# Performance work log

Measured on AMD Instinct MI355X. Metric: run time of the kernel, lower is better.

The kernel has to match this reference:

```python
import jax, jax.numpy as jnp
import numpy as np

B, N, F_NODE = 16, 48, 5
H1, H2 = 32, 64
D_ATT = H2 * 3  # 192


def setup_inputs() -> dict:
    rng = np.random.default_rng(0)
    n_nodes = B * N
    # complete graph per batch element; each directed pair appears with class 0 and class 1,
    # ordered by (src, dst, class) so that filtering src>dst leaves a sorted list where
    # consecutive rows are the (class0, class1) pair of the same undirected edge.
    i, j = np.meshgrid(np.arange(N), np.arange(N), indexing="ij")
    m = i != j
    pi = np.repeat(i[m], 2)
    pj = np.repeat(j[m], 2)
    cls = np.tile(np.array([0.0, 1.0], np.float32), N * (N - 1))
    offs = np.arange(B)[:, None] * N
    src = (pi[None] + offs).ravel()
    dst = (pj[None] + offs).ravel()
    edges = jnp.asarray(np.stack([src, dst]).astype(np.int64))
    w = rng.random(src.shape[0]).astype(np.float32)
    edge_attr = jnp.asarray(np.stack([w, np.tile(cls, B)], axis=1))
    x = jnp.asarray(rng.standard_normal((n_nodes, F_NODE)).astype(np.float32))
    detector_labels = jnp.ones((n_nodes,), bool)
    batch_labels = jnp.asarray(np.repeat(np.arange(B), N).astype(np.int64))

    def lin(k_out, k_in):
        s = 1.0 / np.sqrt(k_in)
        return (jnp.asarray(rng.uniform(-s, s, (k_out, k_in)).astype(np.float32)),
                jnp.asarray(rng.uniform(-s, s, (k_out,)).astype(np.float32)))

    W_we, b_we = lin(1, 3)
    Wrel1, brel1 = lin(H1, F_NODE); Wroot1, _ = lin(H1, F_NODE)
    Wrel2, brel2 = lin(H2, H1);     Wroot2, _ = lin(H2, H1)
    W_ee, b_ee = lin(H2, 3)
    W_qkv, b_qkv = lin(3 * D_ATT, D_ATT)
    W_in, b_in = lin(3 * D_ATT, D_ATT)
    W_out, b_out = lin(D_ATT, D_ATT)
    W_o, b_o = lin(1, D_ATT)
    return dict(x=x, edges=edges, edge_attr=edge_attr,
                detector_labels=detector_labels, batch_labels=batch_labels,
                W_we=W_we, b_we=b_we, Wrel1=Wrel1, brel1=brel1, Wroot1=Wroot1,
                Wrel2=Wrel2, brel2=brel2, Wroot2=Wroot2,
                W_ee=W_ee, b_ee=b_ee, W_qkv=W_qkv, b_qkv=b_qkv,
                W_in=W_in, b_in=b_in, W_out=W_out, b_out=b_out,
                W_o=W_o, b_o=b_o)


def _graph_conv(x, src, dst, w, Wrel, brel, Wroot, n_nodes):
    # pyg GraphConv: lin_rel(sum_{j->i} e_ji * x_j) + lin_root(x_i)
    msg = x[src] * w  # w: [E,1] scalar edge weight
    agg = jax.ops.segment_sum(msg, dst, num_segments=n_nodes)
    return agg @ Wrel.T + brel + x @ Wroot.T


def reference(x, edges, edge_attr, detector_labels, batch_labels,
              W_we, b_we, Wrel1, brel1, Wroot1, Wrel2, brel2, Wroot2,
              W_ee, b_ee, W_qkv, b_qkv, W_in, b_in, W_out, b_out, W_o, b_o):
    n_nodes = x.shape[0]
    E = edges.shape[1]
    src, dst = edges[0], edges[1]
    # edge weight embedding from (weight, one_hot(class))
    c = jax.nn.one_hot(edge_attr[:, 1].astype(jnp.int32), 2, dtype=x.dtype)
    w = jax.nn.relu(jnp.concatenate([edge_attr[:, :1], c], -1) @ W_we.T + b_we)  # [E,1]
    x = jax.nn.relu(_graph_conv(x, src, dst, w, Wrel1, brel1, Wroot1, n_nodes))
    x = jax.nn.relu(_graph_conv(x, src, dst, w, Wrel2, brel2, Wroot2, n_nodes))
    # keep one direction (src > dst): construction guarantees exactly E//2 kept, already sorted
    keep = jnp.nonzero(src > dst, size=E // 2)[0]
    srcK, dstK, ea = src[keep], dst[keep], edge_attr[keep]
    c = jax.nn.one_hot(ea[:, 1].astype(jnp.int32), 2, dtype=x.dtype)
    wK = jax.nn.relu(jnp.concatenate([ea[:, :1], c], -1) @ W_ee.T + b_ee)  # [Ek,H2]
    feat = jnp.concatenate([x[srcK], wK, x[dstK]], -1)  # [Ek, 3*H2]
    # equal-size graphs -> unbatch + pad_sequence == reshape (no padding)
    S = feat.shape[0] // B
    feat = feat.reshape(B, S, -1)
    e_src = srcK.reshape(B, S)
    e_dst = dstK.reshape(B, S)
    classes = ea[:, 1].reshape(B, S, 1)
    pad_mask = e_src == e_dst  # all False (no ragged padding here)
    # SelfAttention: extra qkv projection, then 1-head MultiheadAttention
    qkv = feat @ W_qkv.T + b_qkv
    q, k, v = jnp.split(qkv, 3, -1)
    Wq, Wk, Wv = jnp.split(W_in, 3, 0)
    bq, bk, bv = jnp.split(b_in, 3, 0)
    q = q @ Wq.T + bq; k = k @ Wk.T + bk; v = v @ Wv.T + bv
    scores = jnp.einsum("bqd,bkd->bqk", q, k) / jnp.sqrt(jnp.asarray(q.shape[-1], q.dtype))
    scores = jnp.where(pad_mask[:, None, :], -jnp.inf, scores)
    attn = jax.nn.softmax(scores, -1)
    feat = jnp.einsum("bqk,bkd->bqd", attn, v) @ W_out.T + b_out
    # SplitSyndromes with all-True detector_labels keeps every edge (identity)
    logit = feat @ W_o.T + b_o  # [B,S,1]
    pair = jnp.concatenate([logit[:, ::2], logit[:, 1::2]], -1)   # [B,S/2,2]
    cls2 = jnp.concatenate([classes[:, ::2], classes[:, 1::2]], -1)
    min_inds = jnp.argmin(pair, axis=2, keepdims=True)
    ef = jnp.take_along_axis(pair, min_inds, 2)   # min values, [B,S/2,1]
    ec = jnp.take_along_axis(cls2, min_inds, 2)
    e4s = jnp.stack([e_src[:, ::2], e_src[:, 1::2]], -1)  # [B,S/2,2]
    e4t = jnp.stack([e_dst[:, ::2], e_dst[:, 1::2]], -1)
    out_src = jnp.take_along_axis(e4s, min_inds, -1)
    out_dst = jnp.take_along_axis(e4t, min_inds, -1)
    out_edges = jnp.concatenate([out_src, out_dst], -1)
    return out_edges, ef, ec
```

## Files before the change

kernel.cpp:

```cpp
#include <hip/hip_runtime.h>
#include <hip/hip_bf16.h>

typedef __hip_bfloat16 bf16;
typedef __attribute__((ext_vector_type(8))) short short8;
typedef __attribute__((ext_vector_type(16))) float float16v;
typedef __attribute__((ext_vector_type(2))) float float2v;

#define B_     16
#define N_     48
#define NODES  768
#define PAIRS  2256
#define EK     36096
#define S_     2256
#define SH     1128
#define D_     192
#define KITERS 71
#define QTILES 71
#define KPB    6144
#define QSCALE 0.10411754f

__device__ __forceinline__ float bf(const bf16* p, int i) { return __bfloat162float(p[i]); }
__device__ __forceinline__ float u2f(unsigned short u) {
    return __uint_as_float(((unsigned int)u) << 16);
}
__device__ __forceinline__ float sanitize(float v) {
    if (v > -1e4f && v < 1e4f) return v;
    if (v >= 1e4f) return 1e4f;
    if (v <= -1e4f) return -1e4f;
    return 0.f;
}

__global__ __launch_bounds__(256) void stage1_kernel(
    const bf16* edge_attr, const bf16* W_we, const bf16* b_we, const bf16* x,
    const bf16* Wrel1, const bf16* brel1, const bf16* Wroot1,
    const bf16* Wrel2, const bf16* brel2, const bf16* Wroot2,
    const bf16* W_o, const bf16* b_o, const bf16* W_out, const bf16* b_out,
    const bf16* W_in, const bf16* b_in, const bf16* b_qkv, const bf16* W_qkv,
    float* x2out, float* wo_eff, float* bq_eff, float* bk_eff, float* bv_eff, float* sc,
    float* WqT, float* WkT, bf16* W2b) {
    int blk = blockIdx.x, tid = threadIdx.x;
    if (blk < 16) {
        int b = blk;
        __shared__ float s_ws[N_ * N_];
        __shared__ float s_x[N_ * 5], s_agg1[N_ * 5];
        __shared__ float s_x1[N_ * 32], s_agg2[N_ * 32];
        float we0 = bf(W_we, 0), we1 = bf(W_we, 1), we2 = bf(W_we, 2), bw = bf(b_we, 0);
        for (int idx = tid; idx < N_ * N_; idx += 256) {
            int i = idx / N_, j = idx % N_;
            float v = 0.f;
            if (i != j) {
                int p = i * 47 + (j < i ? j : j - 1);
                int e = (b * PAIRS + p) * 2;
                float w0 = fmaxf(we0 * bf(edge_attr, (e + 0) * 2) + we1 + bw, 0.f);
                float w1 = fmaxf(we0 * bf(edge_attr, (e + 1) * 2) + we2 + bw, 0.f);
                v = w0 + w1;
            }
            s_ws[idx] = v;
        }
        for (int idx = tid; idx < N_ * 5; idx += 256) s_x[idx] = bf(x, b * N_ * 5 + idx);
        __syncthreads();
        if (tid < 240) {
            int j = tid / 5, f = tid % 5;
            float a = 0.f;
            for (int i = 0; i < N_; i++) a += s_ws[i * N_ + j] * s_x[i * 5 + f];
            s_agg1[tid] = a;
        }
        __syncthreads();
        for (int o = tid; o < N_ * 32; o += 256) {
            int j = o >> 5, h = o & 31;
            float a = bf(brel1, h);
            for (int f = 0; f < 5; f++)
                a += bf(Wrel1, h * 5 + f) * s_agg1[j * 5 + f] +
                     bf(Wroot1, h * 5 + f) * s_x[j * 5 + f];
            s_x1[o] = fmaxf(a, 0.f);
        }
        __syncthreads();
        for (int o = tid; o < N_ * 32; o += 256) {
            int j = o >> 5, h = o & 31;
            float a = 0.f;
            for (int i = 0; i < N_; i++) a += s_ws[i * N_ + j] * s_x1[i * 32 + h];
            s_agg2[o] = a;
        }
        __syncthreads();
        for (int o = tid; o < N_ * 64; o += 256) {
            int j = o >> 6, h2 = o & 63;
            float a = bf(brel2, h2);
            for (int h1 = 0; h1 < 32; h1++)
                a += bf(Wrel2, h2 * 32 + h1) * s_agg2[j * 32 + h1] +
                     bf(Wroot2, h2 * 32 + h1) * s_x1[j * 32 + h1];
            x2out[(b * N_ + j) * 64 + h2] = fmaxf(a, 0.f);
        }
    } else if (blk < 209) {
        int a = blk - 16;
        int wave = tid >> 6, lane = tid & 63;
        float partial = 0.f;
        if (a < 192) {
            if (wave == 0) {
                for (int m = lane; m < 192; m += 64)
                    partial += bf(W_o, m) * bf(W_out, m * 192 + a);
            } else {
                int row = (wave - 1) * 192 + a;
                for (int m = lane; m < 192; m += 64)
                    partial += bf(W_in, row * 192 + m) * bf(b_qkv, (wave - 1) * 192 + m);
            }
        } else if (wave == 0) {
            for (int m = lane; m < 192; m += 64) partial += bf(W_o, m) * bf(b_out, m);
        }
        for (int off = 32; off; off >>= 1) partial += __shfl_xor(partial, off, 64);
        if (lane == 0) {
            if (a < 192) {
                if (wave == 0) wo_eff[a] = partial;
                else if (wave == 1) bq_eff[a] = partial + bf(b_in, a);
                else if (wave == 2) bk_eff[a] = partial + bf(b_in, 192 + a);
                else bv_eff[a] = partial + bf(b_in, 384 + a);
            } else if (wave == 0) sc[1] = partial + bf(b_o, 0);
        }
    } else {
        int idx = (blk - 209) * 256 + tid;
        if (idx < D_ * D_) {
            int a = idx / D_, c = idx % D_;
            float acc = 0.f;
            for (int m = 0; m < D_; m++) acc += bf(W_in, a * D_ + m) * bf(W_qkv, m * D_ + c);
            WqT[c * D_ + a] = acc;
            if (c >= 64 && c < 128) W2b[a * 64 + (c - 64)] = __float2bfloat16(acc);
        } else {
            int t = idx - D_ * D_, a = t / D_, c = t % D_;
            float acc = 0.f;
            for (int m = 0; m < D_; m++)
                acc += bf(W_in, (D_ + a) * D_ + m) * bf(W_qkv, (D_ + m) * D_ + c);
            WkT[c * D_ + a] = acc;
            if (c >= 64 && c < 128) W2b[(192 + a) * 64 + (c - 64)] = __float2bfloat16(acc);
        }
    }
}

__global__ __launch_bounds__(256) void stage2_kernel(
    const bf16* W_in, const bf16* W_qkv, const float* wo_eff, const float* bv_eff,
    const float* x2, const float* WqT, const float* WkT,
    const float* bq_eff, const float* bk_eff,
    float* wvl, float* sc, float* Tq1, float* Tq3, float* Tk1, float* Tk3) {
    int blk = blockIdx.x, tid = threadIdx.x;
    if (blk == 0) {
        if (tid < 64) {
            float partial = 0.f;
            for (int aa = tid; aa < 192; aa += 64) partial += wo_eff[aa] * bv_eff[aa];
            for (int off = 32; off; off >>= 1) partial += __shfl_xor(partial, off, 64);
            if (tid == 0) sc[0] = partial;
        }
    } else if (blk < 193) {
        int w = blk - 1;
        __shared__ float s_tm[192];
        if (tid < 192) {
            float tm = 0.f;
            for (int aa = 0; aa < 192; aa++)
                tm += wo_eff[aa] * bf(W_in, (384 + aa) * 192 + tid);
            s_tm[tid] = tm;
        }
        __syncthreads();
        if (tid < 64) {
            float partial = 0.f;
            for (int m = tid; m < 192; m += 64)
                partial += s_tm[m] * bf(W_qkv, (384 + m) * 192 + w);
            for (int off = 32; off; off >>= 1) partial += __shfl_xor(partial, off, 64);
            if (tid == 0) wvl[w] = partial;
        }
    } else {
        int n = blk - 193;
        __shared__ float sx[64];
        if (tid < 64) sx[tid] = x2[n * 64 + tid];
        __syncthreads();
        if (tid < D_) {
            int a = tid;
            float q1 = bq_eff[a], q3 = 0.f, k1 = bk_eff[a], k3 = 0.f;
            for (int c = 0; c < 64; c++) {
                float xv = sx[c];
                q1 += WqT[c * D_ + a] * xv;
                q3 += WqT[(128 + c) * D_ + a] * xv;
                k1 += WkT[c * D_ + a] * xv;
                k3 += WkT[(128 + c) * D_ + a] * xv;
            }
            Tq1[n * D_ + a] = q1; Tq3[n * D_ + a] = q3;
            Tk1[n * D_ + a] = k1; Tk3[n * D_ + a] = k3;
        }
    }
}

__global__ __launch_bounds__(256) void qkvmid_kernel(
    const bf16* edge_attr, const bf16* W_ee, const bf16* b_ee, const bf16* W2b,
    const float* wvl, const float* sc, const float* x2,
    const float* Tq1, const float* Tq3, const float* Tk1, const float* Tk3,
    bf16* Q, bf16* Kp, float* vl) {
    __shared__ short s_wk[32 * 72];
    __shared__ float s_wvl[192];
    __shared__ int s_ni[32], s_nj[32], s_koff[32];
    __shared__ float s_wraw[32], s_cls[32];
    int tid = threadIdx.x, base = blockIdx.x * 32;
    int wave = tid >> 6, lane = tid & 63;
    int l5 = lane & 31, h5 = lane >> 5;

    short8 bfr[3][4];
    #pragma unroll
    for (int tt = 0; tt < 3; tt++) {
        int ta = wave + tt * 4;
        const short* wrow = (const short*)W2b + (ta * 32 + l5) * 64;
        #pragma unroll
        for (int kc = 0; kc < 4; kc++)
            bfr[tt][kc] = *(const short8*)(wrow + kc * 16 + h5 * 8);
    }

    if (tid < 192) s_wvl[tid] = wvl[tid];
    if (tid < 32) {
        int kk_g = base + tid;
        int b = kk_g / S_, kk = kk_g % S_;
        int q = kk >> 1, cls = kk & 1;
        int i = (int)((1.0f + sqrtf(8.0f * (float)q + 1.0f)) * 0.5f);
        while (i * (i - 1) / 2 > q) --i;
        while ((i + 1) * i / 2 <= q) ++i;
        int j = q - i * (i - 1) / 2;
        s_ni[tid] = b * N_ + i; s_nj[tid] = b * N_ + j;
        int e = (b * PAIRS + i * 47 + j) * 2 + cls;
        s_wraw[tid] = bf(edge_attr, e * 2);
        s_cls[tid] = (float)cls;
        s_koff[tid] = (b * KITERS + (kk >> 5)) * KPB + (kk & 31) * 8;
    }
    __syncthreads();
    for (int idx = tid; idx < 32 * 64; idx += 256) {
        int t = idx >> 6, h = idx & 63;
        int cls = (int)s_cls[t];
        float v = bf(W_ee, h * 3) * s_wraw[t] + bf(W_ee, h * 3 + 1 + cls) + bf(b_ee, h);
        bf16 bv = __float2bfloat16(fmaxf(v, 0.f));
        s_wk[t * 72 + h] = *reinterpret_cast<short*>(&bv);
    }
    __syncthreads();

    short8 af[4];
    #pragma unroll
    for (int kc = 0; kc < 4; kc++)
        af[kc] = *(const short8*)&s_wk[l5 * 72 + kc * 16 + h5 * 8];

    int tl[16], niv[16], njv[16];
    #pragma unroll
    for (int r = 0; r < 16; r++) {
        int t = (r & 3) + 8 * (r >> 2) + 4 * h5;
        tl[r] = t; niv[r] = s_ni[t]; njv[r] = s_nj[t];
    }

    #pragma unroll
    for (int tt = 0; tt < 3; tt++) {
        int ta = wave + tt * 4;
        bool isq = ta < 6;
        int ag = (isq ? ta : ta - 6) * 32 + l5;
        float16v c;
        #pragma unroll
        for (int r = 0; r < 16; r++) c[r] = 0.f;
        #pragma unroll
        for (int kc = 0; kc < 4; kc++)
            c = __builtin_amdgcn_mfma_f32_32x32x16_bf16(af[kc], bfr[tt][kc], c, 0, 0, 0);
        const float* T1 = isq ? Tq1 : Tk1;
        const float* T3 = isq ? Tq3 : Tk3;
        if (isq) {
            #pragma unroll
            for (int r = 0; r < 16; r++) {
                float v = (c[r] + T1[niv[r] * D_ + ag] + T3[njv[r] * D_ + ag]) * QSCALE;
                Q[(long)(base + tl[r]) * D_ + ag] = __float2bfloat16(v);
            }
        } else {
            int kc = ag >> 4, h5w = (ag >> 3) & 1, e = ag & 7;
            int coff = kc * 512 + h5w * 256 + e;
            #pragma unroll
            for (int r = 0; r < 16; r++) {
                float v = c[r] + T1[niv[r] * D_ + ag] + T3[njv[r] * D_ + ag];
                Kp[s_koff[tl[r]] + coff] = __float2bfloat16(v);
            }
        }
    }
    {
        int t = tid >> 3, g = tid & 7;
        const float* xi = &x2[s_ni[t] * 64];
        const float* xj = &x2[s_nj[t] * 64];
        float v = 0.f;
        #pragma unroll
        for (int hh = 0; hh < 8; hh++) {
            int h = g * 8 + hh;
            v += s_wvl[h] * xi[h] + s_wvl[128 + h] * xj[h] +
                 s_wvl[64 + h] * u2f((unsigned short)s_wk[t * 72 + h]);
        }
        v += __shfl_xor(v, 1, 64);
        v += __shfl_xor(v, 2, 64);
        v += __shfl_xor(v, 4, 64);
        if (g == 0) vl[base + t] = v + sc[0];
    }
}

__global__ __launch_bounds__(256) void attn_kernel(const bf16* Q, const bf16* Kp,
                                                   const float* vl, float* part) {
    int x = blockIdx.x;
    int rr = x & 7, rest = x >> 3;
    int hi = rest >= 144;
    int b = rr + 8 * hi;
    int s = rest - 144 * hi;
    int chunk = s / 18, qg = s % 18;
    int tid = threadIdx.x;
    int wave = tid >> 6, lane = tid & 63;
    int n5 = lane & 31, h5 = lane >> 5;
    int qt = qg * 4 + wave;
    bool qvalid = qt < QTILES;
    int t0 = chunk * 9;
    int nit = (chunk == 7) ? 8 : 9;

    short8 qf[12];
    {
        int qrow = b * S_ + qt * 32 + n5;
        if (qrow > B_ * S_ - 1) qrow = B_ * S_ - 1;
        const short* qp = (const short*)Q + (long)qrow * D_;
        #pragma unroll
        for (int kc = 0; kc < 12; kc++) qf[kc] = *(const short8*)(qp + kc * 16 + h5 * 8);
    }

    float lr[16], ar[16];
    #pragma unroll
    for (int r = 0; r < 16; r++) { lr[r] = 0.f; ar[r] = 0.f; }

    const short* Kb = (const short*)Kp + (long)b * KITERS * KPB + h5 * 256 + n5 * 8;
    const float* vlb = vl + b * S_;

    for (int k = 0; k < nit; ++k) {
        int it = t0 + k;
        const short* kp = Kb + it * KPB;
        short8 bfr[12];
        #pragma unroll
        for (int kc = 0; kc < 12; kc++) bfr[kc] = *(const short8*)(kp + kc * 512);
        int row = it * 32 + n5;
        float vlv = vlb[row < S_ ? row : S_ - 1];
        float16v c;
        #pragma unroll
        for (int r = 0; r < 16; r++) c[r] = 0.f;
        #pragma unroll
        for (int kc = 0; kc < 12; kc++)
            c = __builtin_amdgcn_mfma_f32_32x32x16_bf16(qf[kc], bfr[kc], c, 0, 0, 0);
        if (it != KITERS - 1) {
            #pragma unroll
            for (int r = 0; r < 16; r++) {
                float p = __builtin_amdgcn_exp2f(c[r]);
                lr[r] += p;
                ar[r] += p * vlv;
            }
        } else {
            bool kv = n5 < 16;
            #pragma unroll
            for (int r = 0; r < 16; r++) {
                float p = kv ? __builtin_amdgcn_exp2f(c[r]) : 0.f;
                lr[r] += p;
                ar[r] += p * vlv;
            }
        }
    }

    if (qvalid) {
        #pragma unroll
        for (int r = 0; r < 16; r++) {
            float l = lr[r], a = ar[r];
            #pragma unroll
            for (int off = 1; off < 32; off <<= 1) {
                l += __shfl_xor(l, off, 64);
                a += __shfl_xor(a, off, 64);
            }
            if (n5 == 0) {
                int qrow = qt * 32 + (r & 3) + 8 * (r >> 2) + 4 * h5;
                if (qrow < S_) {
                    float2v pv2 = {l, a};
                    *(float2v*)&part[((long)(b * S_ + qrow) * 8 + chunk) * 2] = pv2;
                }
            }
        }
    }
}

__global__ __launch_bounds__(256) void final_kernel(const float* part, const float* sc,
                                                    float* out) {
    int idx = blockIdx.x * 256 + threadIdx.x;
    if (idx >= B_ * SH) return;
    int b = idx / SH, p = idx % SH;
    int i = (int)((1.0f + sqrtf(8.0f * (float)p + 1.0f)) * 0.5f);
    while (i * (i - 1) / 2 > p) --i;
    while ((i + 1) * i / 2 <= p) ++i;
    int j = p - i * (i - 1) / 2;
    float co = sc[1];
    float lg[2];
    #pragma unroll
    for (int t = 0; t < 2; t++) {
        long g = (long)b * S_ + 2 * p + t;
        float l = 0.f, a = 0.f;
        #pragma unroll
        for (int c = 0; c < 8; c++) {
            float2v pc = *(const float2v*)&part[(g * 8 + c) * 2];
            l += pc.x;
            a += pc.y;
        }
        lg[t] = sanitize(a / l + co);
    }
    int ind = (lg[1] < lg[0]) ? 1 : 0;
    float ef = ind ? lg[1] : lg[0];
    out[(b * SH + p) * 2 + 0] = (float)(b * N_ + i);
    out[(b * SH + p) * 2 + 1] = (float)(b * N_ + j);
    out[2 * B_ * SH + idx] = ef;
    out[2 * B_ * SH + B_ * SH + idx] = (float)ind;
}

extern "C" void kernel_launch(void* const* d_in, const int* in_sizes, int n_in,
                              void* d_out, int out_size, void* d_ws, size_t ws_size,
                              hipStream_t stream) {
    const bf16* x         = (const bf16*)d_in[0];
    const bf16* edge_attr = (const bf16*)d_in[2];
    const bf16* W_we   = (const bf16*)d_in[5];
    const bf16* b_we   = (const bf16*)d_in[6];
    const bf16* Wrel1  = (const bf16*)d_in[7];
    const bf16* brel1  = (const bf16*)d_in[8];
    const bf16* Wroot1 = (const bf16*)d_in[9];
    const bf16* Wrel2  = (const bf16*)d_in[10];
    const bf16* brel2  = (const bf16*)d_in[11];
    const bf16* Wroot2 = (const bf16*)d_in[12];
    const bf16* W_ee   = (const bf16*)d_in[13];
    const bf16* b_ee   = (const bf16*)d_in[14];
    const bf16* W_qkv  = (const bf16*)d_in[15];
    const bf16* b_qkv  = (const bf16*)d_in[16];
    const bf16* W_in   = (const bf16*)d_in[17];
    const bf16* b_in   = (const bf16*)d_in[18];
    const bf16* W_out  = (const bf16*)d_in[19];
    const bf16* b_out  = (const bf16*)d_in[20];
    const bf16* W_o    = (const bf16*)d_in[21];
    const bf16* b_o    = (const bf16*)d_in[22];

    float* w = (float*)d_ws;
    float* WqT    = w;
    float* WkT    = WqT + 36864;
    float* bq_eff = WkT + 36864;
    float* bk_eff = bq_eff + 192;
    float* bv_eff = bk_eff + 192;
    float* wo_eff = bv_eff + 192;
    float* wvl    = wo_eff + 192;
    float* sc     = wvl + 192;
    float* x2     = sc + 64;
    float* vl     = x2 + 49152;
    float* part   = vl + 36096;
    bf16*  Q      = (bf16*)(part + 577536);
    bf16*  Kp     = Q + (long)EK * D_;
    bf16*  W2b    = Kp + (long)B_ * KITERS * KPB;
    float* Tq1    = (float*)(W2b + 384 * 64);
    float* Tq3    = Tq1 + NODES * D_;
    float* Tk1    = Tq3 + NODES * D_;
    float* Tk3    = Tk1 + NODES * D_;

    stage1_kernel<<<497, 256, 0, stream>>>(edge_attr, W_we, b_we, x, Wrel1, brel1, Wroot1,
                                           Wrel2, brel2, Wroot2, W_o, b_o, W_out, b_out,
                                           W_in, b_in, b_qkv, W_qkv,
                                           x2, wo_eff, bq_eff, bk_eff, bv_eff, sc,
                                           WqT, WkT, W2b);
    stage2_kernel<<<961, 256, 0, stream>>>(W_in, W_qkv, wo_eff, bv_eff, x2, WqT, WkT,
                                           bq_eff, bk_eff, wvl, sc, Tq1, Tq3, Tk1, Tk3);
    qkvmid_kernel<<<EK / 32, 256, 0, stream>>>(edge_attr, W_ee, b_ee, W2b, wvl, sc, x2,
                                               Tq1, Tq3, Tk1, Tk3, Q, Kp, vl);
    attn_kernel<<<2304, 256, 0, stream>>>(Q, Kp, vl, part);
    final_kernel<<<(B_ * SH + 255) / 256, 256, 0, stream>>>(part, sc, (float*)d_out);
}
```

Measured before the change: 246.1 us.

## Process two query tiles per wave to reuse K fragments, split attention launch

Each wave now computes two 32-row query tiles against every K tile it loads, so each loaded K fragment feeds two MFMAs and K traffic per query is halved. The grid shrinks from 2304 to 576 blocks per launch, and the attention kernel is launched twice, once for chunks 0-3 and once for chunks 4-7. This doubles the per-thread registers for Q fragments and accumulators, which can lower occupancy, and adds one extra kernel launch.

```diff
diff --git a/kernel.cpp b/kernel.cpp
--- a/kernel.cpp
+++ b/kernel.cpp
@@ -293,33 +293,40 @@
 }
 
 __global__ __launch_bounds__(256) void attn_kernel(const bf16* Q, const bf16* Kp,
-                                                   const float* vl, float* part) {
+                                                   const float* vl, float* part,
+                                                   int chunk0) {
     int x = blockIdx.x;
     int rr = x & 7, rest = x >> 3;
-    int hi = rest >= 144;
+    int hi = rest >= 36;
     int b = rr + 8 * hi;
-    int s = rest - 144 * hi;
-    int chunk = s / 18, qg = s % 18;
+    int s = rest - 36 * hi;
+    int chunk = chunk0 + s / 9, qg = s % 9;
     int tid = threadIdx.x;
     int wave = tid >> 6, lane = tid & 63;
     int n5 = lane & 31, h5 = lane >> 5;
-    int qt = qg * 4 + wave;
-    bool qvalid = qt < QTILES;
+    int qtA = qg * 8 + wave * 2;
+    int qtB = qtA + 1;
+    bool validB = qtB < QTILES;
     int t0 = chunk * 9;
     int nit = (chunk == 7) ? 8 : 9;
 
-    short8 qf[12];
+    short8 qfA[12], qfB[12];
     {
-        int qrow = b * S_ + qt * 32 + n5;
-        if (qrow > B_ * S_ - 1) qrow = B_ * S_ - 1;
-        const short* qp = (const short*)Q + (long)qrow * D_;
-        #pragma unroll
-        for (int kc = 0; kc < 12; kc++) qf[kc] = *(const short8*)(qp + kc * 16 + h5 * 8);
-    }
-
-    float lr[16], ar[16];
-    #pragma unroll
-    for (int r = 0; r < 16; r++) { lr[r] = 0.f; ar[r] = 0.f; }
+        int qrowA = b * S_ + qtA * 32 + n5;
+        int qrowB = b * S_ + qtB * 32 + n5;
+        if (qrowB > B_ * S_ - 1) qrowB = B_ * S_ - 1;
+        const short* qpA = (const short*)Q + (long)qrowA * D_;
+        const short* qpB = (const short*)Q + (long)qrowB * D_;
+        #pragma unroll
+        for (int kc = 0; kc < 12; kc++) {
+            qfA[kc] = *(const short8*)(qpA + kc * 16 + h5 * 8);
+            qfB[kc] = *(const short8*)(qpB + kc * 16 + h5 * 8);
+        }
+    }
+
+    float lrA[16], arA[16], lrB[16], arB[16];
+    #pragma unroll
+    for (int r = 0; r < 16; r++) { lrA[r] = 0.f; arA[r] = 0.f; lrB[r] = 0.f; arB[r] = 0.f; }
 
     const short* Kb = (const short*)Kp + (long)b * KITERS * KPB + h5 * 256 + n5 * 8;
     const float* vlb = vl + b * S_;
@@ -327,46 +334,62 @@
     for (int k = 0; k < nit; ++k) {
         int it = t0 + k;
         const short* kp = Kb + it * KPB;
-        short8 bfr[12];
-        #pragma unroll
-        for (int kc = 0; kc < 12; kc++) bfr[kc] = *(const short8*)(kp + kc * 512);
         int row = it * 32 + n5;
         float vlv = vlb[row < S_ ? row : S_ - 1];
-        float16v c;
-        #pragma unroll
-        for (int r = 0; r < 16; r++) c[r] = 0.f;
-        #pragma unroll
-        for (int kc = 0; kc < 12; kc++)
-            c = __builtin_amdgcn_mfma_f32_32x32x16_bf16(qf[kc], bfr[kc], c, 0, 0, 0);
+        float16v cA, cB;
+        #pragma unroll
+        for (int r = 0; r < 16; r++) { cA[r] = 0.f; cB[r] = 0.f; }
+        #pragma unroll
+        for (int kc = 0; kc < 12; kc++) {
+            short8 bfr = *(const short8*)(kp + kc * 512);
+            cA = __builtin_amdgcn_mfma_f32_32x32x16_bf16(qfA[kc], bfr, cA, 0, 0, 0);
+            cB = __builtin_amdgcn_mfma_f32_32x32x16_bf16(qfB[kc], bfr, cB, 0, 0, 0);
+        }
         if (it != KITERS - 1) {
             #pragma unroll
             for (int r = 0; r < 16; r++) {
-                float p = __builtin_amdgcn_exp2f(c[r]);
-                lr[r] += p;
-                ar[r] += p * vlv;
+                float pA = __builtin_amdgcn_exp2f(cA[r]);
+                float pB = __builtin_amdgcn_exp2f(cB[r]);
+                lrA[r] += pA; arA[r] += pA * vlv;
+                lrB[r] += pB; arB[r] += pB * vlv;
             }
         } else {
             bool kv = n5 < 16;
             #pragma unroll
             for (int r = 0; r < 16; r++) {
-                float p = kv ? __builtin_amdgcn_exp2f(c[r]) : 0.f;
-                lr[r] += p;
-                ar[r] += p * vlv;
-            }
-        }
-    }
-
-    if (qvalid) {
+                float pA = kv ? __builtin_amdgcn_exp2f(cA[r]) : 0.f;
+                float pB = kv ? __builtin_amdgcn_exp2f(cB[r]) : 0.f;
+                lrA[r] += pA; arA[r] += pA * vlv;
+                lrB[r] += pB; arB[r] += pB * vlv;
+            }
+        }
+    }
+
+    #pragma unroll
+    for (int r = 0; r < 16; r++) {
+        float l = lrA[r], a = arA[r];
+        #pragma unroll
+        for (int off = 1; off < 32; off <<= 1) {
+            l += __shfl_xor(l, off, 64);
+            a += __shfl_xor(a, off, 64);
+        }
+        if (n5 == 0) {
+            int qrow = qtA * 32 + (r & 3) + 8 * (r >> 2) + 4 * h5;
+            float2v pv2 = {l, a};
+            *(float2v*)&part[((long)(b * S_ + qrow) * 8 + chunk) * 2] = pv2;
+        }
+    }
+    if (validB) {
         #pragma unroll
         for (int r = 0; r < 16; r++) {
-            float l = lr[r], a = ar[r];
+            float l = lrB[r], a = arB[r];
             #pragma unroll
             for (int off = 1; off < 32; off <<= 1) {
                 l += __shfl_xor(l, off, 64);
                 a += __shfl_xor(a, off, 64);
             }
             if (n5 == 0) {
-                int qrow = qt * 32 + (r & 3) + 8 * (r >> 2) + 4 * h5;
+                int qrow = qtB * 32 + (r & 3) + 8 * (r >> 2) + 4 * h5;
                 if (qrow < S_) {
                     float2v pv2 = {l, a};
                     *(float2v*)&part[((long)(b * S_ + qrow) * 8 + chunk) * 2] = pv2;
@@ -460,6 +483,7 @@
                                            bq_eff, bk_eff, wvl, sc, Tq1, Tq3, Tk1, Tk3);
     qkvmid_kernel<<<EK / 32, 256, 0, stream>>>(edge_attr, W_ee, b_ee, W2b, wvl, sc, x2,
                                                Tq1, Tq3, Tk1, Tk3, Q, Kp, vl);
-    attn_kernel<<<2304, 256, 0, stream>>>(Q, Kp, vl, part);
+    attn_kernel<<<576, 256, 0, stream>>>(Q, Kp, vl, part, 0);
+    attn_kernel<<<576, 256, 0, stream>>>(Q, Kp, vl, part, 4);
     final_kernel<<<(B_ * SH + 255) / 256, 256, 0, stream>>>(part, sc, (float*)d_out);
 }
```

After: 312.8 us. +27.1%, slower.
